# Optimization experiments

Measured on AMD Instinct MI355X. Metric: run time of the kernel, lower is better.

Reference implementation:

```python
import jax, jax.numpy as jnp
import numpy as np

EPS = 1e-5
K_SIZE, STRIDE, DILATION, N_HEADS = 8, 2, 2, 8


def ln2d(x, w, b):
    # LayerNorm2d: normalize over channel axis of NCHW
    m = x.mean(1, keepdims=True)
    v = x.var(1, keepdims=True)
    return (x - m) * jax.lax.rsqrt(v + EPS) * w[None, :, None, None] + b[None, :, None, None]


def setup_inputs() -> dict:
    key = jax.random.key(0)
    ks = jax.random.split(key, 8)
    B, C, H, W = 1, 64, 128, 128
    hid = 2 * C  # ffn_ratio = 2
    f = lambda k, s: jax.random.normal(k, s, jnp.float32) * 0.02
    return dict(
        x=jax.random.normal(ks[0], (B, C, H, W), jnp.float32),
        norm1_w=jnp.ones(C, jnp.float32), norm1_b=jnp.zeros(C, jnp.float32),
        qkv_w=f(ks[1], (3 * C, C)), qkv_b=jnp.zeros(3 * C, jnp.float32),
        qn_w=jnp.ones(C, jnp.float32), qn_b=jnp.zeros(C, jnp.float32),
        kn_w=jnp.ones(C, jnp.float32), kn_b=jnp.zeros(C, jnp.float32),
        proj_w=f(ks[2], (C, C)), proj_b=jnp.zeros(C, jnp.float32),
        gamma1=jnp.full((C,), 0.1, jnp.float32),
        norm2_w=jnp.ones(C, jnp.float32), norm2_b=jnp.zeros(C, jnp.float32),
        fc1_w=f(ks[3], (hid, C)), fc1_b=jnp.zeros(hid, jnp.float32),
        mn_w=jnp.ones(hid, jnp.float32), mn_b=jnp.zeros(hid, jnp.float32),
        fc2_w=f(ks[4], (C, hid)), fc2_b=jnp.zeros(C, jnp.float32),
        gamma2=jnp.full((C,), 0.1, jnp.float32),
    )


def reference(x, norm1_w, norm1_b, qkv_w, qkv_b, qn_w, qn_b, kn_w, kn_b,
              proj_w, proj_b, gamma1, norm2_w, norm2_b,
              fc1_w, fc1_b, mn_w, mn_b, fc2_w, fc2_b, gamma2):
    B, C, H, W = x.shape
    n = N_HEADS
    hd = C // n
    # strided + dilated neighborhood offsets (includes 0 at center)
    off = (jnp.arange(K_SIZE) * STRIDE - (K_SIZE * STRIDE) // 2) * DILATION

    # ---- neighborhood attention branch ----
    xn = ln2d(x, norm1_w, norm1_b)
    qkv = jnp.einsum('oc,bchw->bohw', qkv_w, xn) + qkv_b[None, :, None, None]
    q, k, v = jnp.split(qkv, 3, axis=1)
    q = ln2d(q, qn_w, qn_b)
    k = ln2d(k, kn_w, kn_b)
    q = q.reshape(B, n, hd, H, W)
    k = k.reshape(B, n, hd, H, W)
    v = v.reshape(B, n, hd, H, W)

    pos_h = jnp.arange(H)[:, None] + off[None, :]            # [H, k]
    vh = (pos_h >= 0) & (pos_h < H)
    ih = jnp.clip(pos_h, 0, H - 1)
    pos_w = jnp.arange(W)[:, None] + off[None, :]            # [W, k]
    vw = (pos_w >= 0) & (pos_w < W)
    iw = jnp.clip(pos_w, 0, W - 1)

    # gather neighborhoods: [B,n,hd,H,kh,W,kw]
    Kg = jnp.take(jnp.take(k, ih, axis=3), iw, axis=5)
    Vg = jnp.take(jnp.take(v, ih, axis=3), iw, axis=5)

    scores = jnp.einsum('bnchw,bnchiwj->bnhwij', q, Kg) * (hd ** -0.5)
    mask = vh[:, None, :, None] & vw[None, :, None, :]        # [H,W,kh,kw]
    scores = jnp.where(mask[None, None], scores, -jnp.inf)
    a = jax.nn.softmax(scores.reshape(B, n, H, W, -1), axis=-1).reshape(scores.shape)
    o = jnp.einsum('bnhwij,bnchiwj->bnchw', a, Vg).reshape(B, C, H, W)
    o = jnp.einsum('oc,bchw->bohw', proj_w, o) + proj_b[None, :, None, None]
    x = x + gamma1[None, :, None, None] * o                  # ls1 + residual (drop_path=0)

    # ---- ConvMlp branch: 1x1 conv -> norm -> silu -> 1x1 conv ----
    y = ln2d(x, norm2_w, norm2_b)
    h1 = jnp.einsum('oc,bchw->bohw', fc1_w, y) + fc1_b[None, :, None, None]
    h1 = jax.nn.silu(ln2d(h1, mn_w, mn_b))
    h2 = jnp.einsum('oc,bchw->bohw', fc2_w, h1) + fc2_b[None, :, None, None]
    return x + gamma2[None, :, None, None] * h2
```

## Files before the change

### kernel.cpp

```cpp
#include <hip/hip_runtime.h>
#include <math.h>

#define HW 16384
#define CC 64
#define HID 128
#define EPSV 1e-5f
#define ROW 36
#define QROW 205
#define HDSTR 131072


__global__ __launch_bounds__(256) void k_ln_qkv(
    const float* __restrict__ x,
    const float* __restrict__ n1w, const float* __restrict__ n1b,
    const float* __restrict__ qkvw, const float* __restrict__ qkvb,
    const float* __restrict__ qnw, const float* __restrict__ qnb,
    const float* __restrict__ knw, const float* __restrict__ knb,
    float* __restrict__ qo, float* __restrict__ ko, float* __restrict__ vo)
{
    __shared__ __align__(16) float xs[CC][ROW];
    __shared__ __align__(16) float qk[32][QROW];
    __shared__ __align__(16) float mu1[32], rs1[32], muq[32], rsq[32], muk[32], rsk[32];

    const int t = threadIdx.x;
    const int pix0 = blockIdx.x * 32;

    {
        const int c = t >> 2, pxq = (t & 3) * 8;
        *(float4*)&xs[c][pxq]     = *(const float4*)(x + c * HW + pix0 + pxq);
        *(float4*)&xs[c][pxq + 4] = *(const float4*)(x + c * HW + pix0 + pxq + 4);
    }
    __syncthreads();

    if (t < 128) {
        const int px = ((t >> 6) << 4) + (t & 15);
        const int part = (t & 63) >> 4;
        float s = 0.f, ss = 0.f;
        #pragma unroll
        for (int i = 0; i < 16; ++i) { float v = xs[part * 16 + i][px]; s += v; ss += v * v; }
        s += __shfl_xor(s, 16); ss += __shfl_xor(ss, 16);
        s += __shfl_xor(s, 32); ss += __shfl_xor(ss, 32);
        if (part == 0) {
            float m = s * (1.f / CC);
            mu1[px] = m;
            rs1[px] = rsqrtf(ss * (1.f / CC) - m * m + EPSV);
        }
    }
    __syncthreads();

    {
        const int c = t >> 2, pxq = (t & 3) * 8;
        const float wgt = n1w[c], bia = n1b[c];
        #pragma unroll
        for (int hh = 0; hh < 2; ++hh) {
            float4 v = *(float4*)&xs[c][pxq + hh * 4];
            float4 m4 = *(float4*)&mu1[pxq + hh * 4];
            float4 r4 = *(float4*)&rs1[pxq + hh * 4];
            v.x = (v.x - m4.x) * r4.x * wgt + bia;
            v.y = (v.y - m4.y) * r4.y * wgt + bia;
            v.z = (v.z - m4.z) * r4.z * wgt + bia;
            v.w = (v.w - m4.w) * r4.w * wgt + bia;
            *(float4*)&xs[c][pxq + hh * 4] = v;
        }
    }
    __syncthreads();

    {
        const int o0 = (t >> 3) * 6;
        const int px0 = (t & 7) * 4;
        float a[6][4];
        #pragma unroll
        for (int j = 0; j < 6; ++j) {
            float b = qkvb[o0 + j];
            a[j][0] = b; a[j][1] = b; a[j][2] = b; a[j][3] = b;
        }
        for (int c = 0; c < CC; c += 4) {
            float4 xv[4];
            #pragma unroll
            for (int i = 0; i < 4; ++i) xv[i] = *(float4*)&xs[c + i][px0];
            #pragma unroll
            for (int j = 0; j < 6; ++j) {
                float4 wv = *(const float4*)(qkvw + (o0 + j) * CC + c);
                #pragma unroll
                for (int pp = 0; pp < 4; ++pp) {
                    float xv0 = (&xv[0].x)[pp], xv1 = (&xv[1].x)[pp];
                    float xv2 = (&xv[2].x)[pp], xv3 = (&xv[3].x)[pp];
                    a[j][pp] += wv.x * xv0 + wv.y * xv1 + wv.z * xv2 + wv.w * xv3;
                }
            }
        }
        #pragma unroll
        for (int j = 0; j < 6; ++j) {
            #pragma unroll
            for (int pp = 0; pp < 4; ++pp) qk[px0 + pp][o0 + j] = a[j][pp];
        }
    }
    __syncthreads();

    if (t < 128) {
        const int px = ((t >> 6) << 4) + (t & 15);
        const int part = (t & 63) >> 4;
        float s = 0.f, ss = 0.f;
        #pragma unroll
        for (int i = 0; i < 16; ++i) { float v = qk[px][part * 16 + i]; s += v; ss += v * v; }
        s += __shfl_xor(s, 16); ss += __shfl_xor(ss, 16);
        s += __shfl_xor(s, 32); ss += __shfl_xor(ss, 32);
        if (part == 0) {
            float m = s * (1.f / CC);
            muq[px] = m;
            rsq[px] = rsqrtf(ss * (1.f / CC) - m * m + EPSV);
        }
    } else {
        const int t2 = t - 128;
        const int px = ((t2 >> 6) << 4) + (t2 & 15);
        const int part = (t2 & 63) >> 4;
        float s = 0.f, ss = 0.f;
        #pragma unroll
        for (int i = 0; i < 16; ++i) { float v = qk[px][CC + part * 16 + i]; s += v; ss += v * v; }
        s += __shfl_xor(s, 16); ss += __shfl_xor(ss, 16);
        s += __shfl_xor(s, 32); ss += __shfl_xor(ss, 32);
        if (part == 0) {
            float m = s * (1.f / CC);
            muk[px] = m;
            rsk[px] = rsqrtf(ss * (1.f / CC) - m * m + EPSV);
        }
    }
    __syncthreads();

    #pragma unroll
    for (int pass = 0; pass < 2; ++pass) {
        const int px = (t >> 4) + pass * 16;
        const int cg = t & 15;
        const int c = cg * 4;
        const int hd = cg >> 1;
        const int d4 = (cg & 1) * 4;
        const int pixel = pix0 + px;
        const int h = pixel >> 7, w = pixel & 127;
        const int pos = ((h >> 2) * 32 + (w >> 2)) * 16 + (h & 3) * 4 + (w & 3);
        const int gbase = hd * HDSTR + pos * 8 + d4;

        const float mq = muq[px], rq = rsq[px];
        float4 qv = *(float4*)&qk[px][c];
        float4 qw = *(const float4*)(qnw + c);
        float4 qb = *(const float4*)(qnb + c);
        qv.x = (qv.x - mq) * rq * qw.x + qb.x;
        qv.y = (qv.y - mq) * rq * qw.y + qb.y;
        qv.z = (qv.z - mq) * rq * qw.z + qb.z;
        qv.w = (qv.w - mq) * rq * qw.w + qb.w;
        *(float4*)(qo + gbase) = qv;

        const float mk = muk[px], rk = rsk[px];
        float4 kv = *(float4*)&qk[px][CC + c];
        float4 kw = *(const float4*)(knw + c);
        float4 kb = *(const float4*)(knb + c);
        kv.x = (kv.x - mk) * rk * kw.x + kb.x;
        kv.y = (kv.y - mk) * rk * kw.y + kb.y;
        kv.z = (kv.z - mk) * rk * kw.z + kb.z;
        kv.w = (kv.w - mk) * rk * kw.w + kb.w;
        *(float4*)(ko + gbase) = kv;

        float4 vv = *(float4*)&qk[px][2 * CC + c];
        *(float4*)(vo + gbase) = vv;
    }
}

__global__ __launch_bounds__(256) void k_attn(
    const float* __restrict__ q, const float* __restrict__ k, const float* __restrict__ v,
    float* __restrict__ o)
{
    __shared__ __align__(16) float kt[4][15][33][2];
    __shared__ __align__(16) float vt[4][15][33][2];

    const int t = threadIdx.x;
    const int band = blockIdx.x;
    const int sub  = blockIdx.y;
    const int head = blockIdx.z;
    const int hs0 = band * 8;

    const float* kb = k + head * HDSTR;
    const float* vb = v + head * HDSTR;

    for (int idx = t; idx < 960; idx += 256) {
        const int row = idx >> 6;
        const int rem = idx & 63;
        const int ws = rem >> 1;
        const int dh = rem & 1;
        int gr = hs0 - 4 + row;
        gr = gr < 0 ? 0 : (gr > 31 ? 31 : gr);
        const int gaddr = ((gr * 32 + ws) * 16 + sub) * 8 + dh * 4;
        const float4 kv4 = *(const float4*)(kb + gaddr);
        const float4 vv4 = *(const float4*)(vb + gaddr);
        const int dp = dh * 2;
        kt[dp][row][ws][0] = kv4.x;     kt[dp][row][ws][1] = kv4.y;
        kt[dp + 1][row][ws][0] = kv4.z; kt[dp + 1][row][ws][1] = kv4.w;
        vt[dp][row][ws][0] = vv4.x;     vt[dp][row][ws][1] = vv4.y;
        vt[dp + 1][row][ws][0] = vv4.z; vt[dp + 1][row][ws][1] = vv4.w;
    }

    const int r = t >> 5;
    const int ws = t & 31;
    const int hs = hs0 + r;

    const float* qp = q + head * HDSTR + ((hs * 32 + ws) * 16 + sub) * 8;
    const float4 q0 = *(const float4*)qp;
    const float4 q1 = *(const float4*)(qp + 4);
    const float scale = 0.35355339059327373f;

    __syncthreads();

    float s[64];
    float mx0 = -1e30f, mx1 = -1e30f, mx2 = -1e30f, mx3 = -1e30f;
    #pragma unroll
    for (int i = 0; i < 8; ++i) {
        const int lr = r + i;
        const bool vh = (unsigned)(hs + i - 4) < 32u;
        #pragma unroll
        for (int j = 0; j < 8; ++j) {
            const int cs = ws + j - 4;
            const bool valid = vh && ((unsigned)cs < 32u);
            const int cc = cs < 0 ? 0 : (cs > 31 ? 31 : cs);
            const float2 kA = *(const float2*)&kt[0][lr][cc][0];
            const float2 kB = *(const float2*)&kt[1][lr][cc][0];
            const float2 kC = *(const float2*)&kt[2][lr][cc][0];
            const float2 kD = *(const float2*)&kt[3][lr][cc][0];
            float sv = q0.x * kA.x + q0.y * kA.y + q0.z * kB.x + q0.w * kB.y
                     + q1.x * kC.x + q1.y * kC.y + q1.z * kD.x + q1.w * kD.y;
            sv *= scale;
            sv = valid ? sv : -INFINITY;
            s[i * 8 + j] = sv;
            if ((j & 3) == 0)      mx0 = fmaxf(mx0, sv);
            else if ((j & 3) == 1) mx1 = fmaxf(mx1, sv);
            else if ((j & 3) == 2) mx2 = fmaxf(mx2, sv);
            else                   mx3 = fmaxf(mx3, sv);
        }
    }
    const float mx = fmaxf(fmaxf(mx0, mx1), fmaxf(mx2, mx3));

    float l = 0.f;
    float a0 = 0.f, a1 = 0.f, a2 = 0.f, a3 = 0.f, a4 = 0.f, a5 = 0.f, a6 = 0.f, a7 = 0.f;
    #pragma unroll
    for (int i = 0; i < 8; ++i) {
        const int lr = r + i;
        #pragma unroll
        for (int j = 0; j < 8; ++j) {
            const int cs = ws + j - 4;
            const int cc = cs < 0 ? 0 : (cs > 31 ? 31 : cs);
            const float p = __expf(s[i * 8 + j] - mx);
            const float2 vA = *(const float2*)&vt[0][lr][cc][0];
            const float2 vB = *(const float2*)&vt[1][lr][cc][0];
            const float2 vC = *(const float2*)&vt[2][lr][cc][0];
            const float2 vD = *(const float2*)&vt[3][lr][cc][0];
            l += p;
            a0 += p * vA.x;  a1 += p * vA.y;
            a2 += p * vB.x;  a3 += p * vB.y;
            a4 += p * vC.x;  a5 += p * vC.y;
            a6 += p * vD.x;  a7 += p * vD.y;
        }
    }

    const float inv = 1.f / l;
    const int a = sub >> 2, b = sub & 3;
    const int h = hs * 4 + a, w = ws * 4 + b;
    float* op = o + (h * 128 + w) * 64 + head * 8;
    float4 r0 = {a0 * inv, a1 * inv, a2 * inv, a3 * inv};
    float4 r1 = {a4 * inv, a5 * inv, a6 * inv, a7 * inv};
    *(float4*)op = r0;
    *(float4*)(op + 4) = r1;
}

__global__ __launch_bounds__(256) void k_mlp(
    const float* __restrict__ x, const float* __restrict__ oatt,
    const float* __restrict__ pw, const float* __restrict__ pb,
    const float* __restrict__ g1,
    const float* __restrict__ n2w, const float* __restrict__ n2b,
    const float* __restrict__ f1w, const float* __restrict__ f1b,
    const float* __restrict__ mnw, const float* __restrict__ mnb,
    const float* __restrict__ f2w, const float* __restrict__ f2b,
    const float* __restrict__ g2,
    float* __restrict__ out)
{
    __shared__ __align__(16) float xres[CC][ROW];
    __shared__ __align__(16) float tb[CC][ROW];
    __shared__ __align__(16) float h1[HID][ROW];
    __shared__ __align__(16) float mu[32], rs[32];

    const int t = threadIdx.x;
    const int pix0 = blockIdx.x * 32;

    {
        const int c = t >> 2, pxq = (t & 3) * 8;
        *(float4*)&xres[c][pxq]     = *(const float4*)(x + c * HW + pix0 + pxq);
        *(float4*)&xres[c][pxq + 4] = *(const float4*)(x + c * HW + pix0 + pxq + 4);
    }
    #pragma unroll
    for (int pass = 0; pass < 2; ++pass) {
        const int px = (t >> 4) + pass * 16, cg = (t & 15) * 4;
        float4 ov = *(const float4*)(oatt + (pix0 + px) * CC + cg);
        tb[cg][px] = ov.x; tb[cg + 1][px] = ov.y; tb[cg + 2][px] = ov.z; tb[cg + 3][px] = ov.w;
    }
    __syncthreads();

    {
        const int o0 = (t >> 3) * 2;
        const int px0 = (t & 7) * 4;
        float a[2][4];
        #pragma unroll
        for (int j = 0; j < 2; ++j) {
            float b = pb[o0 + j];
            a[j][0] = b; a[j][1] = b; a[j][2] = b; a[j][3] = b;
        }
        for (int c = 0; c < CC; c += 4) {
            float4 xv[4];
            #pragma unroll
            for (int i = 0; i < 4; ++i) xv[i] = *(float4*)&tb[c + i][px0];
            #pragma unroll
            for (int j = 0; j < 2; ++j) {
                float4 wv = *(const float4*)(pw + (o0 + j) * CC + c);
                #pragma unroll
                for (int pp = 0; pp < 4; ++pp) {
                    a[j][pp] += wv.x * (&xv[0].x)[pp] + wv.y * (&xv[1].x)[pp]
                              + wv.z * (&xv[2].x)[pp] + wv.w * (&xv[3].x)[pp];
                }
            }
        }
        #pragma unroll
        for (int j = 0; j < 2; ++j) {
            const float gg = g1[o0 + j];
            #pragma unroll
            for (int pp = 0; pp < 4; ++pp) xres[o0 + j][px0 + pp] += gg * a[j][pp];
        }
    }
    __syncthreads();

    if (t < 128) {
        const int px = ((t >> 6) << 4) + (t & 15);
        const int part = (t & 63) >> 4;
        float s = 0.f, ss = 0.f;
        #pragma unroll
        for (int i = 0; i < 16; ++i) { float v = xres[part * 16 + i][px]; s += v; ss += v * v; }
        s += __shfl_xor(s, 16); ss += __shfl_xor(ss, 16);
        s += __shfl_xor(s, 32); ss += __shfl_xor(ss, 32);
        if (part == 0) {
            float m = s * (1.f / CC);
            mu[px] = m;
            rs[px] = rsqrtf(ss * (1.f / CC) - m * m + EPSV);
        }
    }
    __syncthreads();

    {
        const int c = t >> 2, pxq = (t & 3) * 8;
        const float wgt = n2w[c], bia = n2b[c];
        #pragma unroll
        for (int hh = 0; hh < 2; ++hh) {
            float4 v = *(float4*)&xres[c][pxq + hh * 4];
            float4 m4 = *(float4*)&mu[pxq + hh * 4];
            float4 r4 = *(float4*)&rs[pxq + hh * 4];
            v.x = (v.x - m4.x) * r4.x * wgt + bia;
            v.y = (v.y - m4.y) * r4.y * wgt + bia;
            v.z = (v.z - m4.z) * r4.z * wgt + bia;
            v.w = (v.w - m4.w) * r4.w * wgt + bia;
            *(float4*)&tb[c][pxq + hh * 4] = v;
        }
    }
    __syncthreads();

    {
        const int o0 = (t >> 3) * 4;
        const int px0 = (t & 7) * 4;
        float a[4][4];
        #pragma unroll
        for (int j = 0; j < 4; ++j) {
            float b = f1b[o0 + j];
            a[j][0] = b; a[j][1] = b; a[j][2] = b; a[j][3] = b;
        }
        for (int c = 0; c < CC; c += 4) {
            float4 xv[4];
            #pragma unroll
            for (int i = 0; i < 4; ++i) xv[i] = *(float4*)&tb[c + i][px0];
            #pragma unroll
            for (int j = 0; j < 4; ++j) {
                float4 wv = *(const float4*)(f1w + (o0 + j) * CC + c);
                #pragma unroll
                for (int pp = 0; pp < 4; ++pp) {
                    a[j][pp] += wv.x * (&xv[0].x)[pp] + wv.y * (&xv[1].x)[pp]
                              + wv.z * (&xv[2].x)[pp] + wv.w * (&xv[3].x)[pp];
                }
            }
        }
        #pragma unroll
        for (int j = 0; j < 4; ++j) {
            #pragma unroll
            for (int pp = 0; pp < 4; ++pp) h1[o0 + j][px0 + pp] = a[j][pp];
        }
    }
    __syncthreads();

    if (t < 128) {
        const int px = ((t >> 6) << 4) + (t & 15);
        const int part = (t & 63) >> 4;
        float s = 0.f, ss = 0.f;
        #pragma unroll
        for (int i = 0; i < 32; ++i) { float v = h1[part * 32 + i][px]; s += v; ss += v * v; }
        s += __shfl_xor(s, 16); ss += __shfl_xor(ss, 16);
        s += __shfl_xor(s, 32); ss += __shfl_xor(ss, 32);
        if (part == 0) {
            float m = s * (1.f / HID);
            mu[px] = m;
            rs[px] = rsqrtf(ss * (1.f / HID) - m * m + EPSV);
        }
    }
    __syncthreads();

    {
        const int c = t >> 1, ph = (t & 1) * 16;
        const float wgt = mnw[c], bia = mnb[c];
        #pragma unroll
        for (int qq = 0; qq < 4; ++qq) {
            float4 v = *(float4*)&h1[c][ph + qq * 4];
            float4 m4 = *(float4*)&mu[ph + qq * 4];
            float4 r4 = *(float4*)&rs[ph + qq * 4];
            float hv;
            hv = (v.x - m4.x) * r4.x * wgt + bia; v.x = hv / (1.f + __expf(-hv));
            hv = (v.y - m4.y) * r4.y * wgt + bia; v.y = hv / (1.f + __expf(-hv));
            hv = (v.z - m4.z) * r4.z * wgt + bia; v.z = hv / (1.f + __expf(-hv));
            hv = (v.w - m4.w) * r4.w * wgt + bia; v.w = hv / (1.f + __expf(-hv));
            *(float4*)&h1[c][ph + qq * 4] = v;
        }
    }
    __syncthreads();

    {
        const int o0 = (t >> 3) * 2;
        const int px0 = (t & 7) * 4;
        float a[2][4];
        #pragma unroll
        for (int j = 0; j < 2; ++j) {
            float b = f2b[o0 + j];
            a[j][0] = b; a[j][1] = b; a[j][2] = b; a[j][3] = b;
        }
        for (int c = 0; c < HID; c += 4) {
            float4 xv[4];
            #pragma unroll
            for (int i = 0; i < 4; ++i) xv[i] = *(float4*)&h1[c + i][px0];
            #pragma unroll
            for (int j = 0; j < 2; ++j) {
                float4 wv = *(const float4*)(f2w + (o0 + j) * HID + c);
                #pragma unroll
                for (int pp = 0; pp < 4; ++pp) {
                    a[j][pp] += wv.x * (&xv[0].x)[pp] + wv.y * (&xv[1].x)[pp]
                              + wv.z * (&xv[2].x)[pp] + wv.w * (&xv[3].x)[pp];
                }
            }
        }
        #pragma unroll
        for (int j = 0; j < 2; ++j) {
            const float gg = g2[o0 + j];
            float4 xr = *(float4*)&xres[o0 + j][px0];
            float4 ov = {xr.x + gg * a[j][0], xr.y + gg * a[j][1],
                         xr.z + gg * a[j][2], xr.w + gg * a[j][3]};
            *(float4*)(out + (o0 + j) * HW + pix0 + px0) = ov;
        }
    }
}

extern "C" void kernel_launch(void* const* d_in, const int* in_sizes, int n_in,
                              void* d_out, int out_size, void* d_ws, size_t ws_size,
                              hipStream_t stream) {
    (void)in_sizes; (void)n_in; (void)out_size; (void)ws_size;
    const float* x      = (const float*)d_in[0];
    const float* n1w    = (const float*)d_in[1];
    const float* n1b    = (const float*)d_in[2];
    const float* qkvw   = (const float*)d_in[3];
    const float* qkvb   = (const float*)d_in[4];
    const float* qnw    = (const float*)d_in[5];
    const float* qnb    = (const float*)d_in[6];
    const float* knw    = (const float*)d_in[7];
    const float* knb    = (const float*)d_in[8];
    const float* pw     = (const float*)d_in[9];
    const float* pb     = (const float*)d_in[10];
    const float* g1     = (const float*)d_in[11];
    const float* n2w    = (const float*)d_in[12];
    const float* n2b    = (const float*)d_in[13];
    const float* f1w    = (const float*)d_in[14];
    const float* f1b    = (const float*)d_in[15];
    const float* mnw    = (const float*)d_in[16];
    const float* mnb    = (const float*)d_in[17];
    const float* f2w    = (const float*)d_in[18];
    const float* f2b    = (const float*)d_in[19];
    const float* g2     = (const float*)d_in[20];
    float* out = (float*)d_out;

    float* ws = (float*)d_ws;
    const size_t CHW = (size_t)CC * HW;
    float* qo   = ws;
    float* ko   = ws + CHW;
    float* vo   = ws + 2 * CHW;
    float* oatt = ws + 3 * CHW;

    k_ln_qkv<<<dim3(HW / 32), dim3(256), 0, stream>>>(
        x, n1w, n1b, qkvw, qkvb, qnw, qnb, knw, knb, qo, ko, vo);
    k_attn<<<dim3(4, 16, 8), dim3(256), 0, stream>>>(qo, ko, vo, oatt);
    k_mlp<<<dim3(HW / 32), dim3(256), 0, stream>>>(
        x, oatt, pw, pb, g1, n2w, n2b, f1w, f1b, mnw, mnb, f2w, f2b, g2, out);
}
```

Measured before the change: 145.5 us.

## Split QKV projection kernel across a grid dimension selecting q, k, or v

The fused LN+QKV kernel now launches three times as many blocks, with blockIdx.y choosing whether a block computes the q, k or v slice of the projection. Each block produces 64 output channels instead of 192, which shrinks the shared staging buffer and per-thread accumulators and raises parallelism and occupancy. In exchange, the input load and the first LayerNorm are recomputed three times per pixel tile, and the block-uniform branch on sel adds a little control flow.

```diff
diff --git a/kernel.cpp b/kernel.cpp
--- a/kernel.cpp
+++ b/kernel.cpp
@@ -6,7 +6,7 @@
 #define HID 128
 #define EPSV 1e-5f
 #define ROW 36
-#define QROW 205
+#define SROW 69
 #define HDSTR 131072
 
 
@@ -19,11 +19,12 @@
     float* __restrict__ qo, float* __restrict__ ko, float* __restrict__ vo)
 {
     __shared__ __align__(16) float xs[CC][ROW];
-    __shared__ __align__(16) float qk[32][QROW];
-    __shared__ __align__(16) float mu1[32], rs1[32], muq[32], rsq[32], muk[32], rsk[32];
+    __shared__ __align__(16) float qk[32][SROW];
+    __shared__ __align__(16) float mu1[32], rs1[32], mu2[32], rs2[32];
 
     const int t = threadIdx.x;
     const int pix0 = blockIdx.x * 32;
+    const int sel = blockIdx.y;
 
     {
         const int c = t >> 2, pxq = (t & 3) * 8;
@@ -66,12 +67,13 @@
     __syncthreads();
 
     {
-        const int o0 = (t >> 3) * 6;
+        const int o0 = (t >> 3) * 2;
         const int px0 = (t & 7) * 4;
-        float a[6][4];
-        #pragma unroll
-        for (int j = 0; j < 6; ++j) {
-            float b = qkvb[o0 + j];
+        const int ow = sel * 64 + o0;
+        float a[2][4];
+        #pragma unroll
+        for (int j = 0; j < 2; ++j) {
+            float b = qkvb[ow + j];
             a[j][0] = b; a[j][1] = b; a[j][2] = b; a[j][3] = b;
         }
         for (int c = 0; c < CC; c += 4) {
@@ -79,54 +81,44 @@
             #pragma unroll
             for (int i = 0; i < 4; ++i) xv[i] = *(float4*)&xs[c + i][px0];
             #pragma unroll
-            for (int j = 0; j < 6; ++j) {
-                float4 wv = *(const float4*)(qkvw + (o0 + j) * CC + c);
+            for (int j = 0; j < 2; ++j) {
+                float4 wv = *(const float4*)(qkvw + (ow + j) * CC + c);
                 #pragma unroll
                 for (int pp = 0; pp < 4; ++pp) {
-                    float xv0 = (&xv[0].x)[pp], xv1 = (&xv[1].x)[pp];
-                    float xv2 = (&xv[2].x)[pp], xv3 = (&xv[3].x)[pp];
-                    a[j][pp] += wv.x * xv0 + wv.y * xv1 + wv.z * xv2 + wv.w * xv3;
+                    a[j][pp] += wv.x * (&xv[0].x)[pp] + wv.y * (&xv[1].x)[pp]
+                              + wv.z * (&xv[2].x)[pp] + wv.w * (&xv[3].x)[pp];
                 }
             }
         }
         #pragma unroll
-        for (int j = 0; j < 6; ++j) {
+        for (int j = 0; j < 2; ++j) {
             #pragma unroll
             for (int pp = 0; pp < 4; ++pp) qk[px0 + pp][o0 + j] = a[j][pp];
         }
     }
     __syncthreads();
 
-    if (t < 128) {
-        const int px = ((t >> 6) << 4) + (t & 15);
-        const int part = (t & 63) >> 4;
-        float s = 0.f, ss = 0.f;
-        #pragma unroll
-        for (int i = 0; i < 16; ++i) { float v = qk[px][part * 16 + i]; s += v; ss += v * v; }
-        s += __shfl_xor(s, 16); ss += __shfl_xor(ss, 16);
-        s += __shfl_xor(s, 32); ss += __shfl_xor(ss, 32);
-        if (part == 0) {
-            float m = s * (1.f / CC);
-            muq[px] = m;
-            rsq[px] = rsqrtf(ss * (1.f / CC) - m * m + EPSV);
-        }
-    } else {
-        const int t2 = t - 128;
-        const int px = ((t2 >> 6) << 4) + (t2 & 15);
-        const int part = (t2 & 63) >> 4;
-        float s = 0.f, ss = 0.f;
-        #pragma unroll
-        for (int i = 0; i < 16; ++i) { float v = qk[px][CC + part * 16 + i]; s += v; ss += v * v; }
-        s += __shfl_xor(s, 16); ss += __shfl_xor(ss, 16);
-        s += __shfl_xor(s, 32); ss += __shfl_xor(ss, 32);
-        if (part == 0) {
-            float m = s * (1.f / CC);
-            muk[px] = m;
-            rsk[px] = rsqrtf(ss * (1.f / CC) - m * m + EPSV);
-        }
-    }
-    __syncthreads();
-
+    if (sel < 2) {
+        if (t < 128) {
+            const int px = ((t >> 6) << 4) + (t & 15);
+            const int part = (t & 63) >> 4;
+            float s = 0.f, ss = 0.f;
+            #pragma unroll
+            for (int i = 0; i < 16; ++i) { float v = qk[px][part * 16 + i]; s += v; ss += v * v; }
+            s += __shfl_xor(s, 16); ss += __shfl_xor(ss, 16);
+            s += __shfl_xor(s, 32); ss += __shfl_xor(ss, 32);
+            if (part == 0) {
+                float m = s * (1.f / CC);
+                mu2[px] = m;
+                rs2[px] = rsqrtf(ss * (1.f / CC) - m * m + EPSV);
+            }
+        }
+        __syncthreads();
+    }
+
+    const float* lw = (sel == 0) ? qnw : knw;
+    const float* lb = (sel == 0) ? qnb : knb;
+    float* dst = (sel == 0) ? qo : ((sel == 1) ? ko : vo);
     #pragma unroll
     for (int pass = 0; pass < 2; ++pass) {
         const int px = (t >> 4) + pass * 16;
@@ -139,28 +131,17 @@
         const int pos = ((h >> 2) * 32 + (w >> 2)) * 16 + (h & 3) * 4 + (w & 3);
         const int gbase = hd * HDSTR + pos * 8 + d4;
 
-        const float mq = muq[px], rq = rsq[px];
-        float4 qv = *(float4*)&qk[px][c];
-        float4 qw = *(const float4*)(qnw + c);
-        float4 qb = *(const float4*)(qnb + c);
-        qv.x = (qv.x - mq) * rq * qw.x + qb.x;
-        qv.y = (qv.y - mq) * rq * qw.y + qb.y;
-        qv.z = (qv.z - mq) * rq * qw.z + qb.z;
-        qv.w = (qv.w - mq) * rq * qw.w + qb.w;
-        *(float4*)(qo + gbase) = qv;
-
-        const float mk = muk[px], rk = rsk[px];
-        float4 kv = *(float4*)&qk[px][CC + c];
-        float4 kw = *(const float4*)(knw + c);
-        float4 kb = *(const float4*)(knb + c);
-        kv.x = (kv.x - mk) * rk * kw.x + kb.x;
-        kv.y = (kv.y - mk) * rk * kw.y + kb.y;
-        kv.z = (kv.z - mk) * rk * kw.z + kb.z;
-        kv.w = (kv.w - mk) * rk * kw.w + kb.w;
-        *(float4*)(ko + gbase) = kv;
-
-        float4 vv = *(float4*)&qk[px][2 * CC + c];
-        *(float4*)(vo + gbase) = vv;
+        float4 vv = *(float4*)&qk[px][c];
+        if (sel < 2) {
+            const float mm = mu2[px], rr = rs2[px];
+            float4 w4 = *(const float4*)(lw + c);
+            float4 b4 = *(const float4*)(lb + c);
+            vv.x = (vv.x - mm) * rr * w4.x + b4.x;
+            vv.y = (vv.y - mm) * rr * w4.y + b4.y;
+            vv.z = (vv.z - mm) * rr * w4.z + b4.z;
+            vv.w = (vv.w - mm) * rr * w4.w + b4.w;
+        }
+        *(float4*)(dst + gbase) = vv;
     }
 }
 
@@ -498,7 +479,7 @@
     float* vo   = ws + 2 * CHW;
     float* oatt = ws + 3 * CHW;
 
-    k_ln_qkv<<<dim3(HW / 32), dim3(256), 0, stream>>>(
+    k_ln_qkv<<<dim3(HW / 32, 3), dim3(256), 0, stream>>>(
         x, n1w, n1b, qkvw, qkvb, qnw, qnb, knw, knb, qo, ko, vo);
     k_attn<<<dim3(4, 16, 8), dim3(256), 0, stream>>>(qo, ko, vo, oatt);
     k_mlp<<<dim3(HW / 32), dim3(256), 0, stream>>>(
```

Result: no change. 144.4 us (-0.8%).
